# Kernel optimization log

Measured on AMD Instinct MI355X. Metric: run time of the kernel, lower is better.

The kernel has to match this reference:

```python
import jax, jax.numpy as jnp
import numpy as np

N_SAMPLES = 32768
CHANNELS = 128
N_ATOMS = 512
ATOM_SIZE = 512
N_TRANSFERS = 64
TRANSFER_SIZE = 8192
N_EVENTS = 32
N_ROOMS = 8
DILATIONS = (1, 3, 9, 27, 1)
BATCH = 8


def _conv1d(x, w, padding, dil=1):
    # x: [B,C,T], w: [O,I,K]
    return jax.lax.conv_general_dilated(
        x, w, (1,), padding, rhs_dilation=(dil,),
        dimension_numbers=('NCH', 'OIH', 'NCH'))


def _fft_convolve(a, b):
    # linear convolution along last dim, truncated to original length
    n = a.shape[-1]
    af = jnp.fft.rfft(a, n=2 * n)
    bf = jnp.fft.rfft(b, n=2 * n)
    return jnp.fft.irfft(af * bf, n=2 * n)[..., :n]


def _mlp(x, hw, hb, ow, ob):
    # LinearOutputStack: 3 hidden Linear(C,C)+leaky_relu, then Linear(C,out)
    for i in range(hw.shape[0]):
        x = jax.nn.leaky_relu(x @ hw[i] + hb[i], 0.2)
    return x @ ow + ob


def setup_inputs() -> dict:
    key = jax.random.key(0)
    ks = jax.random.split(key, 25)
    s = 0.02
    C = CHANNELS
    return {
        'x': jax.random.normal(ks[0], (BATCH, 1, N_SAMPLES), jnp.float32),
        'bank': jax.random.normal(ks[1], (C, 1, 512), jnp.float32) * s,
        'w_net': jax.random.normal(ks[2], (len(DILATIONS), C, C, 3), jnp.float32) * s,
        'b_net': jnp.zeros((len(DILATIONS), C), jnp.float32),
        'attn_w': jax.random.normal(ks[3], (1, C, 1), jnp.float32) * s,
        'attn_b': jnp.zeros((1,), jnp.float32),
        'atoms_hw': jax.random.normal(ks[4], (3, C, C), jnp.float32) * s,
        'atoms_hb': jnp.zeros((3, C), jnp.float32),
        'atoms_ow': jax.random.normal(ks[5], (C, N_ATOMS), jnp.float32) * s,
        'atoms_ob': jnp.zeros((N_ATOMS,), jnp.float32),
        'trans_hw': jax.random.normal(ks[6], (3, C, C), jnp.float32) * s,
        'trans_hb': jnp.zeros((3, C), jnp.float32),
        'trans_ow': jax.random.normal(ks[7], (C, N_TRANSFERS), jnp.float32) * s,
        'trans_ob': jnp.zeros((N_TRANSFERS,), jnp.float32),
        'amp_hw': jax.random.normal(ks[8], (3, C, C), jnp.float32) * s,
        'amp_hb': jnp.zeros((3, C), jnp.float32),
        'amp_ow': jax.random.normal(ks[9], (C, 1), jnp.float32) * s,
        'amp_ob': jnp.zeros((1,), jnp.float32),
        'atoms_dict': jax.random.uniform(ks[10], (N_ATOMS, ATOM_SIZE), jnp.float32, -1.0, 1.0),
        'transfer_dict': jax.random.normal(ks[11], (N_TRANSFERS, TRANSFER_SIZE), jnp.float32) * 0.01,
        'rooms': jax.random.normal(ks[12], (N_ROOMS, N_SAMPLES), jnp.float32) * 0.01,
        'room_w': jax.random.normal(ks[13], (C, N_ROOMS), jnp.float32) * s,
        'room_b': jnp.zeros((N_ROOMS,), jnp.float32),
        'mix_w': jax.random.normal(ks[14], (C, 1), jnp.float32) * s,
        'mix_b': jnp.zeros((1,), jnp.float32),
    }


def reference(x, bank, w_net, b_net, attn_w, attn_b,
              atoms_hw, atoms_hb, atoms_ow, atoms_ob,
              trans_hw, trans_hb, trans_ow, trans_ob,
              amp_hw, amp_hb, amp_ow, amp_ob,
              atoms_dict, transfer_dict, rooms, room_w, room_b, mix_w, mix_b):
    B = x.shape[0]
    # front-end filter bank, padding=256, truncate to n_samples
    h = _conv1d(x, bank, [(256, 256)])[..., :N_SAMPLES]            # [B,C,T]
    # DilatedStack: residual dilated convs
    for i, d in enumerate(DILATIONS):
        h = h + jax.nn.leaky_relu(
            _conv1d(h, w_net[i], 'SAME', d) + b_net[i][None, :, None], 0.2)
    # ExampleNorm: per-example std normalization
    h = h / (jnp.std(h, axis=(1, 2), keepdims=True) + 1e-8)
    context = jnp.max(h, axis=-1)                                   # [B,C]
    attn = jax.nn.sigmoid(_conv1d(h, attn_w, 'SAME') + attn_b[None, :, None])[:, 0, :]  # [B,T]
    # sparsify_vectors: top-k attention positions, latents scaled by attn
    vals, idx = jax.lax.top_k(attn, N_EVENTS)                        # [B,E]
    lat = jnp.take_along_axis(jnp.swapaxes(h, 1, 2), idx[..., None], axis=1) * vals[..., None]  # [B,E,C]
    atoms = jax.nn.softmax(_mlp(lat, atoms_hw, atoms_hb, atoms_ow, atoms_ob), axis=-1) @ atoms_dict
    transfers = jax.nn.softmax(_mlp(lat, trans_hw, trans_hb, trans_ow, trans_ob), axis=-1) @ transfer_dict
    amps = _mlp(lat, amp_hw, amp_hb, amp_ow, amp_ob) ** 2            # [B,E,1]
    atoms = jnp.pad(atoms, ((0, 0), (0, 0), (0, TRANSFER_SIZE - ATOM_SIZE)))
    ev = (_fft_convolve(atoms, transfers) + atoms) * amps            # [B,E,Ts]
    # overlap-add scatter. NOTE: faithful to the original, which does
    # output[:, :, idx:idx+Ts] += x[i, e] -- every event accumulates into a
    # buffer shared across the whole batch.
    pos = idx.reshape(-1)[:, None] + jnp.arange(TRANSFER_SIZE)[None, :]  # [B*E,Ts]
    buf = jnp.zeros(2 * N_SAMPLES, ev.dtype).at[pos].add(ev.reshape(-1, TRANSFER_SIZE))
    dry = jnp.broadcast_to(buf[:N_SAMPLES][None, :], (B, N_SAMPLES))  # [B,T]
    # ReverbGenerator: context -> room choice + wet/dry mix
    impulse = jax.nn.softmax(context @ room_w + room_b, axis=-1) @ rooms  # [B,T]
    mix = jax.nn.sigmoid(context @ mix_w + mix_b)                     # [B,1]
    wet = _fft_convolve(dry, impulse)
    out = dry * (1.0 - mix) + wet * mix
    return out[:, None, :]
```

## Files before the change

### kernel.cpp

```cpp
#include <hip/hip_runtime.h>
#include <math.h>

#define TSAMP 32768
#define CCH 128
#define NBATCH 8
#define NEV 32
#define NROWS 256
#define NATOMS 512
#define ASIZE 512
#define NTRANS 64
#define TSIZE 8192

#define DRY_SCALE 16777216.0f
#define IMP_SCALE 64.0f
#define WET_DESCALE 9.313225746154785e-10f

#define EPAD(i) ((i) + ((i) >> 5))

typedef _Float16 f16x8 __attribute__((ext_vector_type(8)));
typedef _Float16 f16x4 __attribute__((ext_vector_type(4)));
typedef float f32x4 __attribute__((ext_vector_type(4)));


__global__ void k_zs(double* __restrict__ sums) {
  if (threadIdx.x < 16) sums[threadIdx.x] = 0.0;
}

__global__ __launch_bounds__(256) void k_zero(float* __restrict__ wet,
                                              float* __restrict__ dry) {
  int i = blockIdx.x * 256 + threadIdx.x;
  if (i < NBATCH * TSAMP) wet[i] = 0.f;
  if (i < TSAMP) dry[i] = 0.f;
}

__global__ __launch_bounds__(256) void k_wsplit(const float* __restrict__ wn,
                                                _Float16* __restrict__ whi,
                                                _Float16* __restrict__ wlo) {
  const int i = blockIdx.x * 256 + threadIdx.x;
  if (i >= 245760) return;
  const int ci = i & 127;
  int r = i >> 7;
  const int o = r & 127;
  r >>= 7;
  const int k = r % 3;
  const int l = r / 3;
  const float w = wn[(((size_t)l*128 + o)*128 + ci)*3 + k];
  const _Float16 hi = (_Float16)w;
  whi[i] = hi;
  wlo[i] = (_Float16)(w - (float)hi);
}

__global__ __launch_bounds__(256) void k_bsplit(const float* __restrict__ bank,
                                                _Float16* __restrict__ bhi,
                                                _Float16* __restrict__ blo) {
  const int i = blockIdx.x * 256 + threadIdx.x;
  if (i < 65536) {
    const float w = bank[i];
    const _Float16 hi = (_Float16)w;
    bhi[i] = hi;
    blo[i] = (_Float16)(w - (float)hi);
  }
}

__global__ __launch_bounds__(256) void k_front_mfma(
    const float* __restrict__ x, const _Float16* __restrict__ bhi,
    const _Float16* __restrict__ blo, float* __restrict__ h) {
  __shared__ _Float16 shi[8*664];
  __shared__ _Float16 slo[8*664];
  const int t0 = blockIdx.x * 128;
  const int b  = blockIdx.y;
  const float* xb = x + (size_t)b*TSAMP;
  const int tid = threadIdx.x;

  for (int flat = tid; flat < 8*632; flat += 256) {
    const int p = flat / 632;
    const int q = flat - p*632;
    const int g = t0 - 256 + q + p;
    const float v = (g >= 0 && g < TSAMP) ? xb[g] : 0.f;
    const _Float16 hi = (_Float16)v;
    shi[p*664 + q] = hi;
    slo[p*664 + q] = (_Float16)(v - (float)hi);
  }
  __syncthreads();

  const int wv = tid >> 6;
  const int lane = tid & 63;
  const int n = lane & 15;
  const int quad = lane >> 4;
  const int c0 = wv * 32;
  const int ph = n & 7;
  const int nb = n & 8;

  f32x4 acc[2][8];
#pragma unroll
  for (int i = 0; i < 2; ++i)
#pragma unroll
    for (int j = 0; j < 8; ++j) acc[i][j] = (f32x4){0.f,0.f,0.f,0.f};

  for (int kc = 0; kc < 16; ++kc) {
    const int kb = kc*32 + quad*8;
    f16x8 ahi[2], alo[2];
#pragma unroll
    for (int os = 0; os < 2; ++os) {
      const size_t ao = (size_t)(c0 + os*16 + n)*512 + kb;
      ahi[os] = *(const f16x8*)(bhi + ao);
      alo[os] = *(const f16x8*)(blo + ao);
    }
#pragma unroll
    for (int tg = 0; tg < 2; ++tg) {
      f16x8 xh[4], xl[4];
#pragma unroll
      for (int u = 0; u < 4; ++u) {
        const int a = ph*664 + (tg*4 + u)*16 + nb + kb;
        xh[u] = *(const f16x8*)(shi + a);
        xl[u] = *(const f16x8*)(slo + a);
      }
#pragma unroll
      for (int os = 0; os < 2; ++os)
#pragma unroll
        for (int u = 0; u < 4; ++u) {
          f32x4 a4 = acc[os][tg*4 + u];
          a4 = __builtin_amdgcn_mfma_f32_16x16x32_f16(ahi[os], xh[u], a4, 0, 0, 0);
          a4 = __builtin_amdgcn_mfma_f32_16x16x32_f16(alo[os], xh[u], a4, 0, 0, 0);
          a4 = __builtin_amdgcn_mfma_f32_16x16x32_f16(ahi[os], xl[u], a4, 0, 0, 0);
          acc[os][tg*4 + u] = a4;
        }
    }
  }

  float* hb = h + (size_t)b*TSAMP*CCH;
#pragma unroll
  for (int os = 0; os < 2; ++os) {
    const int cb = c0 + os*16 + quad*4;
#pragma unroll
    for (int ts = 0; ts < 8; ++ts) {
      const int t = t0 + ts*16 + n;
      *(f32x4*)(hb + (size_t)t*CCH + cb) = acc[os][ts];
    }
  }
}

__global__ __launch_bounds__(256) void k_dil_mfma(
    const float* __restrict__ hin0, const _Float16* __restrict__ whi,
    const _Float16* __restrict__ wlo, const float* __restrict__ bias,
    float* __restrict__ hout0, const int d) {
  extern __shared__ _Float16 sh[];
  const int twin = 64 + 2*d;
  _Float16* shi = sh;
  _Float16* slo = sh + twin*136;
  const int t0 = blockIdx.x * 64;
  const size_t bs = (size_t)blockIdx.y * CCH * TSAMP;
  const float* __restrict__ hin = hin0 + bs;
  float* __restrict__ hout = hout0 + bs;
  const int tid = threadIdx.x;

  for (int flat = tid; flat < twin*32; flat += 256) {
    const int tw = flat >> 5;
    const int c4 = (flat & 31) << 2;
    const int g = t0 - d + tw;
    float4 v = {0.f, 0.f, 0.f, 0.f};
    if (g >= 0 && g < TSAMP) v = *(const float4*)(hin + (size_t)g*CCH + c4);
    f16x4 hv, lv;
    hv[0] = (_Float16)v.x; hv[1] = (_Float16)v.y;
    hv[2] = (_Float16)v.z; hv[3] = (_Float16)v.w;
    lv[0] = (_Float16)(v.x - (float)hv[0]); lv[1] = (_Float16)(v.y - (float)hv[1]);
    lv[2] = (_Float16)(v.z - (float)hv[2]); lv[3] = (_Float16)(v.w - (float)hv[3]);
    *(f16x4*)(shi + tw*136 + c4) = hv;
    *(f16x4*)(slo + tw*136 + c4) = lv;
  }
  __syncthreads();

  const int wv = tid >> 6;
  const int lane = tid & 63;
  const int n = lane & 15;
  const int quad = lane >> 4;
  const int o0 = wv * 32;

  f32x4 acc[2][4];
#pragma unroll
  for (int i = 0; i < 2; ++i)
#pragma unroll
    for (int j = 0; j < 4; ++j) acc[i][j] = (f32x4){0.f,0.f,0.f,0.f};

  for (int k = 0; k < 3; ++k) {
    for (int kc = 0; kc < 4; ++kc) {
      const int cib = kc*32 + quad*8;
      f16x8 ahi[2], alo[2];
#pragma unroll
      for (int os = 0; os < 2; ++os) {
        const size_t wo = ((size_t)k*128 + (o0 + os*16 + n))*128 + cib;
        ahi[os] = *(const f16x8*)(whi + wo);
        alo[os] = *(const f16x8*)(wlo + wo);
      }
      f16x8 bhi[4], blo[4];
#pragma unroll
      for (int ts = 0; ts < 4; ++ts) {
        const int a = (ts*16 + n + k*d)*136 + cib;
        bhi[ts] = *(const f16x8*)(shi + a);
        blo[ts] = *(const f16x8*)(slo + a);
      }
#pragma unroll
      for (int os = 0; os < 2; ++os)
#pragma unroll
        for (int ts = 0; ts < 4; ++ts) {
          acc[os][ts] = __builtin_amdgcn_mfma_f32_16x16x32_f16(ahi[os], bhi[ts], acc[os][ts], 0, 0, 0);
          acc[os][ts] = __builtin_amdgcn_mfma_f32_16x16x32_f16(alo[os], bhi[ts], acc[os][ts], 0, 0, 0);
          acc[os][ts] = __builtin_amdgcn_mfma_f32_16x16x32_f16(ahi[os], blo[ts], acc[os][ts], 0, 0, 0);
        }
    }
  }

#pragma unroll
  for (int os = 0; os < 2; ++os) {
    const int ob = o0 + os*16 + quad*4;
    const f32x4 bs4 = *(const f32x4*)(bias + ob);
#pragma unroll
    for (int ts = 0; ts < 4; ++ts) {
      const int t = t0 + ts*16 + n;
      const int tw = ts*16 + n + d;
      const f16x4 phv = *(const f16x4*)(shi + tw*136 + ob);
      const f16x4 plv = *(const f16x4*)(slo + tw*136 + ob);
      f32x4 res;
#pragma unroll
      for (int r = 0; r < 4; ++r) {
        float v = acc[os][ts][r] + bs4[r];
        v = v > 0.f ? v : 0.2f*v;
        res[r] = (float)phv[r] + (float)plv[r] + v;
      }
      *(f32x4*)(hout + (size_t)t*CCH + ob) = res;
    }
  }
}

__global__ __launch_bounds__(256) void k_dil128(
    const float* __restrict__ hin0, const _Float16* __restrict__ whi,
    const _Float16* __restrict__ wlo, const float* __restrict__ bias,
    float* __restrict__ hout0, const int d) {
  extern __shared__ _Float16 sh[];
  const int twin = 128 + 2*d;
  _Float16* shi = sh;
  _Float16* slo = sh + twin*136;
  const int t0 = blockIdx.x * 128;
  const size_t bs = (size_t)blockIdx.y * CCH * TSAMP;
  const float* __restrict__ hin = hin0 + bs;
  float* __restrict__ hout = hout0 + bs;
  const int tid = threadIdx.x;

  for (int flat = tid; flat < twin*32; flat += 256) {
    const int tw = flat >> 5;
    const int c4 = (flat & 31) << 2;
    const int g = t0 - d + tw;
    float4 v = {0.f, 0.f, 0.f, 0.f};
    if (g >= 0 && g < TSAMP) v = *(const float4*)(hin + (size_t)g*CCH + c4);
    f16x4 hv, lv;
    hv[0] = (_Float16)v.x; hv[1] = (_Float16)v.y;
    hv[2] = (_Float16)v.z; hv[3] = (_Float16)v.w;
    lv[0] = (_Float16)(v.x - (float)hv[0]); lv[1] = (_Float16)(v.y - (float)hv[1]);
    lv[2] = (_Float16)(v.z - (float)hv[2]); lv[3] = (_Float16)(v.w - (float)hv[3]);
    *(f16x4*)(shi + tw*136 + c4) = hv;
    *(f16x4*)(slo + tw*136 + c4) = lv;
  }
  __syncthreads();

  const int wv = tid >> 6;
  const int lane = tid & 63;
  const int n = lane & 15;
  const int quad = lane >> 4;
  const int o0 = wv * 32;

  f32x4 acc[2][8];
#pragma unroll
  for (int i = 0; i < 2; ++i)
#pragma unroll
    for (int j = 0; j < 8; ++j) acc[i][j] = (f32x4){0.f,0.f,0.f,0.f};

  for (int k = 0; k < 3; ++k) {
    for (int kc = 0; kc < 4; ++kc) {
      const int cib = kc*32 + quad*8;
      f16x8 ahi[2], alo[2];
#pragma unroll
      for (int os = 0; os < 2; ++os) {
        const size_t wo = ((size_t)k*128 + (o0 + os*16 + n))*128 + cib;
        ahi[os] = *(const f16x8*)(whi + wo);
        alo[os] = *(const f16x8*)(wlo + wo);
      }
#pragma unroll
      for (int tg = 0; tg < 2; ++tg) {
        f16x8 bh[4], bl[4];
#pragma unroll
        for (int u = 0; u < 4; ++u) {
          const int a = ((tg*4 + u)*16 + n + k*d)*136 + cib;
          bh[u] = *(const f16x8*)(shi + a);
          bl[u] = *(const f16x8*)(slo + a);
        }
#pragma unroll
        for (int os = 0; os < 2; ++os)
#pragma unroll
          for (int u = 0; u < 4; ++u) {
            f32x4 a4 = acc[os][tg*4 + u];
            a4 = __builtin_amdgcn_mfma_f32_16x16x32_f16(ahi[os], bh[u], a4, 0, 0, 0);
            a4 = __builtin_amdgcn_mfma_f32_16x16x32_f16(alo[os], bh[u], a4, 0, 0, 0);
            a4 = __builtin_amdgcn_mfma_f32_16x16x32_f16(ahi[os], bl[u], a4, 0, 0, 0);
            acc[os][tg*4 + u] = a4;
          }
      }
    }
  }

#pragma unroll
  for (int os = 0; os < 2; ++os) {
    const int ob = o0 + os*16 + quad*4;
    const f32x4 bs4 = *(const f32x4*)(bias + ob);
#pragma unroll
    for (int ts = 0; ts < 8; ++ts) {
      const int t = t0 + ts*16 + n;
      const int tw = ts*16 + n + d;
      const f16x4 phv = *(const f16x4*)(shi + tw*136 + ob);
      const f16x4 plv = *(const f16x4*)(slo + tw*136 + ob);
      f32x4 res;
#pragma unroll
      for (int r = 0; r < 4; ++r) {
        float v = acc[os][ts][r] + bs4[r];
        v = v > 0.f ? v : 0.2f*v;
        res[r] = (float)phv[r] + (float)plv[r] + v;
      }
      *(f32x4*)(hout + (size_t)t*CCH + ob) = res;
    }
  }
}

__global__ __launch_bounds__(256) void k_dil_last(
    const float* __restrict__ hin0, const _Float16* __restrict__ whi,
    const _Float16* __restrict__ wlo, const float* __restrict__ bias,
    float* __restrict__ hout0, const int d,
    const float* __restrict__ aw, double* __restrict__ sums,
    float* __restrict__ attnraw, float* __restrict__ pm, const int bb0) {
  extern __shared__ _Float16 sh[];
  const int twin = 128 + 2*d;
  _Float16* shi = sh;
  _Float16* slo = sh + twin*136;
  __shared__ float attl[4*128];
  __shared__ double sred[8];
  const int t0 = blockIdx.x * 128;
  const int b = bb0 + blockIdx.y;
  const size_t bs = (size_t)blockIdx.y * CCH * TSAMP;
  const float* __restrict__ hin = hin0 + bs;
  float* __restrict__ hout = hout0 + bs;
  const int tid = threadIdx.x;

  for (int flat = tid; flat < twin*32; flat += 256) {
    const int tw = flat >> 5;
    const int c4 = (flat & 31) << 2;
    const int g = t0 - d + tw;
    float4 v = {0.f, 0.f, 0.f, 0.f};
    if (g >= 0 && g < TSAMP) v = *(const float4*)(hin + (size_t)g*CCH + c4);
    f16x4 hv, lv;
    hv[0] = (_Float16)v.x; hv[1] = (_Float16)v.y;
    hv[2] = (_Float16)v.z; hv[3] = (_Float16)v.w;
    lv[0] = (_Float16)(v.x - (float)hv[0]); lv[1] = (_Float16)(v.y - (float)hv[1]);
    lv[2] = (_Float16)(v.z - (float)hv[2]); lv[3] = (_Float16)(v.w - (float)hv[3]);
    *(f16x4*)(shi + tw*136 + c4) = hv;
    *(f16x4*)(slo + tw*136 + c4) = lv;
  }
  __syncthreads();

  const int wv = tid >> 6;
  const int lane = tid & 63;
  const int n = lane & 15;
  const int quad = lane >> 4;
  const int o0 = wv * 32;

  f32x4 acc[2][8];
#pragma unroll
  for (int i = 0; i < 2; ++i)
#pragma unroll
    for (int j = 0; j < 8; ++j) acc[i][j] = (f32x4){0.f,0.f,0.f,0.f};

  for (int k = 0; k < 3; ++k) {
    for (int kc = 0; kc < 4; ++kc) {
      const int cib = kc*32 + quad*8;
      f16x8 ahi[2], alo[2];
#pragma unroll
      for (int os = 0; os < 2; ++os) {
        const size_t wo = ((size_t)k*128 + (o0 + os*16 + n))*128 + cib;
        ahi[os] = *(const f16x8*)(whi + wo);
        alo[os] = *(const f16x8*)(wlo + wo);
      }
#pragma unroll
      for (int tg = 0; tg < 2; ++tg) {
        f16x8 bh[4], bl[4];
#pragma unroll
        for (int u = 0; u < 4; ++u) {
          const int a = ((tg*4 + u)*16 + n + k*d)*136 + cib;
          bh[u] = *(const f16x8*)(shi + a);
          bl[u] = *(const f16x8*)(slo + a);
        }
#pragma unroll
        for (int os = 0; os < 2; ++os)
#pragma unroll
          for (int u = 0; u < 4; ++u) {
            f32x4 a4 = acc[os][tg*4 + u];
            a4 = __builtin_amdgcn_mfma_f32_16x16x32_f16(ahi[os], bh[u], a4, 0, 0, 0);
            a4 = __builtin_amdgcn_mfma_f32_16x16x32_f16(alo[os], bh[u], a4, 0, 0, 0);
            a4 = __builtin_amdgcn_mfma_f32_16x16x32_f16(ahi[os], bl[u], a4, 0, 0, 0);
            acc[os][tg*4 + u] = a4;
          }
      }
    }
  }

  const f32x4 awq0 = *(const f32x4*)(aw + o0 + quad*4);
  const f32x4 awq1 = *(const f32x4*)(aw + o0 + 16 + quad*4);
  double s = 0.0, s2 = 0.0;
  float pa[8] = {0.f,0.f,0.f,0.f,0.f,0.f,0.f,0.f};
  f32x4 cm[2];
  cm[0] = (f32x4){-3.4e38f, -3.4e38f, -3.4e38f, -3.4e38f};
  cm[1] = cm[0];

#pragma unroll
  for (int os = 0; os < 2; ++os) {
    const int ob = o0 + os*16 + quad*4;
    const f32x4 bs4 = *(const f32x4*)(bias + ob);
    const f32x4 awv = os ? awq1 : awq0;
#pragma unroll
    for (int ts = 0; ts < 8; ++ts) {
      const int t = t0 + ts*16 + n;
      const int tw = ts*16 + n + d;
      const f16x4 phv = *(const f16x4*)(shi + tw*136 + ob);
      const f16x4 plv = *(const f16x4*)(slo + tw*136 + ob);
      f32x4 res;
      float dotp = 0.f;
#pragma unroll
      for (int r = 0; r < 4; ++r) {
        float v = acc[os][ts][r] + bs4[r];
        v = v > 0.f ? v : 0.2f*v;
        const float hv = (float)phv[r] + (float)plv[r] + v;
        res[r] = hv;
        s += (double)hv; s2 += (double)hv*(double)hv;
        dotp += hv * awv[r];
        cm[os][r] = fmaxf(cm[os][r], hv);
      }
      pa[ts] += dotp;
      *(f32x4*)(hout + (size_t)t*CCH + ob) = res;
    }
  }

#pragma unroll
  for (int ts = 0; ts < 8; ++ts) {
    pa[ts] += __shfl_xor(pa[ts], 16);
    pa[ts] += __shfl_xor(pa[ts], 32);
  }
  if (quad == 0) {
#pragma unroll
    for (int ts = 0; ts < 8; ++ts) attl[wv*128 + ts*16 + n] = pa[ts];
  }
#pragma unroll
  for (int mk = 1; mk <= 8; mk <<= 1)
#pragma unroll
    for (int os = 0; os < 2; ++os)
#pragma unroll
      for (int r = 0; r < 4; ++r)
        cm[os][r] = fmaxf(cm[os][r], __shfl_xor(cm[os][r], mk));
  if (n == 0) {
#pragma unroll
    for (int os = 0; os < 2; ++os)
      *(f32x4*)(pm + ((size_t)b*256 + blockIdx.x)*128 + o0 + os*16 + quad*4) = cm[os];
  }
  for (int sft = 32; sft; sft >>= 1) { s += __shfl_down(s, sft); s2 += __shfl_down(s2, sft); }
  if (lane == 0) { sred[wv*2] = s; sred[wv*2+1] = s2; }
  __syncthreads();
  if (tid < 128)
    attnraw[(size_t)b*TSAMP + t0 + tid] =
        attl[tid] + attl[128 + tid] + attl[256 + tid] + attl[384 + tid];
  if (tid == 0) {
    atomicAdd(&sums[b*2],   sred[0] + sred[2] + sred[4] + sred[6]);
    atomicAdd(&sums[b*2+1], sred[1] + sred[3] + sred[5] + sred[7]);
  }
}

__global__ void k_scale(const double* __restrict__ sums, float* __restrict__ scal) {
  const int b = threadIdx.x;
  if (b < NBATCH) {
    const double n = (double)CCH * (double)TSAMP;
    const double mean = sums[b*2] / n;
    double var = sums[b*2+1] / n - mean*mean;
    if (var < 0.0) var = 0.0;
    scal[b] = (float)(1.0 / (sqrt(var) + 1e-8));
  }
}

__global__ void k_context2(const float* __restrict__ pm, const float* __restrict__ scal,
                           float* __restrict__ ctx) {
  const int b = blockIdx.x;
  const int c = threadIdx.x;
  float m = -3.4e38f;
  for (int s = 0; s < 256; ++s) m = fmaxf(m, pm[((size_t)b*256 + s)*128 + c]);
  ctx[b*128 + c] = m * scal[b];
}

__global__ __launch_bounds__(256) void k_topk1(const float* __restrict__ raw,
                                               const float* __restrict__ scal,
                                               const float* __restrict__ ab,
                                               float* __restrict__ cv,
                                               int* __restrict__ cidx) {
  const int ch = blockIdx.x, b = blockIdx.y;
  const float sc = scal[b], bb_ = ab[0];
  const float* a = raw + (size_t)b*TSAMP + ch*2048;
  __shared__ float v[2048];
  __shared__ float rv[4]; __shared__ int ri[4];
  const int tid = threadIdx.x;
  for (int i = tid; i < 2048; i += 256)
    v[i] = 1.f/(1.f+expf(-(a[i]*sc + bb_)));
  __syncthreads();
  for (int e = 0; e < NEV; ++e) {
    float bv = -1e30f; int bi = 0;
    for (int i = tid; i < 2048; i += 256) {
      const float x = v[i];
      if (x > bv) { bv = x; bi = i; }
    }
    for (int s = 32; s; s >>= 1) {
      const float ov = __shfl_down(bv, s); const int oi = __shfl_down(bi, s);
      if (ov > bv || (ov == bv && oi < bi)) { bv = ov; bi = oi; }
    }
    if ((tid & 63) == 0) { rv[tid >> 6] = bv; ri[tid >> 6] = bi; }
    __syncthreads();
    if (tid == 0) {
      int bb = 0;
      for (int w2 = 1; w2 < 4; ++w2)
        if (rv[w2] > rv[bb] || (rv[w2] == rv[bb] && ri[w2] < ri[bb])) bb = w2;
      cv[(b*16 + ch)*NEV + e] = rv[bb];
      cidx[(b*16 + ch)*NEV + e] = ch*2048 + ri[bb];
      v[ri[bb]] = -1e30f;
    }
    __syncthreads();
  }
}

__global__ __launch_bounds__(512) void k_topk2(const float* __restrict__ cv,
                                               const int* __restrict__ ci_,
                                               float* __restrict__ vals,
                                               int* __restrict__ idxs) {
  const int b = blockIdx.x;
  const int tid = threadIdx.x;
  float my = cv[b*512 + tid];
  int   mi = ci_[b*512 + tid];
  __shared__ float rv[8]; __shared__ int ri[8];
  __shared__ float bvs; __shared__ int bis;
  for (int e = 0; e < NEV; ++e) {
    float bv = my; int bi = mi;
    for (int s = 32; s; s >>= 1) {
      const float ov = __shfl_down(bv, s); const int oi = __shfl_down(bi, s);
      if (ov > bv || (ov == bv && oi < bi)) { bv = ov; bi = oi; }
    }
    if ((tid & 63) == 0) { rv[tid >> 6] = bv; ri[tid >> 6] = bi; }
    __syncthreads();
    if (tid == 0) {
      int bb = 0;
      for (int w2 = 1; w2 < 8; ++w2)
        if (rv[w2] > rv[bb] || (rv[w2] == rv[bb] && ri[w2] < ri[bb])) bb = w2;
      vals[b*NEV + e] = rv[bb]; idxs[b*NEV + e] = ri[bb];
      bvs = rv[bb]; bis = ri[bb];
    }
    __syncthreads();
    if (mi == bis && my == bvs) my = -1e30f;
    __syncthreads();
  }
}

__device__ __forceinline__ float blk_max128(float v, float* red) {
  const int tid = threadIdx.x;
  red[tid] = v; __syncthreads();
  for (int s = 64; s > 0; s >>= 1) {
    if (tid < s) red[tid] = fmaxf(red[tid], red[tid + s]);
    __syncthreads();
  }
  const float r = red[0]; __syncthreads();
  return r;
}
__device__ __forceinline__ float blk_sum128(float v, float* red) {
  const int tid = threadIdx.x;
  red[tid] = v; __syncthreads();
  for (int s = 64; s > 0; s >>= 1) {
    if (tid < s) red[tid] += red[tid + s];
    __syncthreads();
  }
  const float r = red[0]; __syncthreads();
  return r;
}
__device__ __forceinline__ float mlp_hidden3(float latv, const float* __restrict__ hw,
                                             const float* __restrict__ hb, float* xa) {
  const int tid = threadIdx.x;
  float cur = latv;
  for (int i = 0; i < 3; ++i) {
    xa[tid] = cur; __syncthreads();
    const float* W = hw + (size_t)i*CCH*CCH;
    float acc = hb[i*CCH + tid];
    for (int c = 0; c < CCH; ++c) acc += xa[c] * W[c*CCH + tid];
    cur = acc > 0.f ? acc : 0.2f*acc;
    __syncthreads();
  }
  return cur;
}

__global__ __launch_bounds__(128) void k_mlp(
    const float* __restrict__ h, const float* __restrict__ scal,
    const float* __restrict__ vals, const int* __restrict__ idxs,
    const float* __restrict__ a_hw, const float* __restrict__ a_hb,
    const float* __restrict__ a_ow, const float* __restrict__ a_ob,
    const float* __restrict__ t_hw, const float* __restrict__ t_hb,
    const float* __restrict__ t_ow, const float* __restrict__ t_ob,
    const float* __restrict__ m_hw, const float* __restrict__ m_hb,
    const float* __restrict__ m_ow, const float* __restrict__ m_ob,
    float* __restrict__ p_atoms, float* __restrict__ p_trans, float* __restrict__ amps) {
  const int row = blockIdx.x;
  const int b = row >> 5;
  const int tid = threadIdx.x;
  __shared__ float xa[CCH];
  __shared__ float red[CCH];
  const int t = idxs[row];
  const float latv = h[((size_t)b*TSAMP + t)*CCH + tid] * scal[b] * vals[row];

  {
    const float cur = mlp_hidden3(latv, a_hw, a_hb, xa);
    xa[tid] = cur; __syncthreads();
    float l0 = a_ob[tid], l1 = a_ob[tid+128], l2 = a_ob[tid+256], l3 = a_ob[tid+384];
    for (int c = 0; c < CCH; ++c) {
      const float xv = xa[c];
      const float* W = a_ow + (size_t)c*NATOMS + tid;
      l0 += xv*W[0]; l1 += xv*W[128]; l2 += xv*W[256]; l3 += xv*W[384];
    }
    const float mx = blk_max128(fmaxf(fmaxf(l0,l1), fmaxf(l2,l3)), red);
    const float e0 = expf(l0-mx), e1 = expf(l1-mx), e2 = expf(l2-mx), e3 = expf(l3-mx);
    const float inv = 1.f / blk_sum128(e0+e1+e2+e3, red);
    float* pa = p_atoms + (size_t)row*NATOMS;
    pa[tid] = e0*inv; pa[tid+128] = e1*inv; pa[tid+256] = e2*inv; pa[tid+384] = e3*inv;
  }
  {
    const float cur = mlp_hidden3(latv, t_hw, t_hb, xa);
    xa[tid] = cur; __syncthreads();
    float lg = -3.4e38f;
    if (tid < NTRANS) {
      float acc = t_ob[tid];
      for (int c = 0; c < CCH; ++c) acc += xa[c]*t_ow[c*NTRANS + tid];
      lg = acc;
    }
    const float mt = blk_max128(lg, red);
    const float et = (tid < NTRANS) ? expf(lg - mt) : 0.f;
    const float st = blk_sum128(et, red);
    if (tid < NTRANS) p_trans[(size_t)row*NTRANS + tid] = et/st;
  }
  {
    const float cur = mlp_hidden3(latv, m_hw, m_hb, xa);
    const float s = blk_sum128(cur * m_ow[tid], red);
    if (tid == 0) { const float v = s + m_ob[0]; amps[row] = v*v; }
  }
}

__global__ __launch_bounds__(256) void k_atoms_mm(const float* __restrict__ p_atoms,
                                                  const float* __restrict__ dict,
                                                  float* __restrict__ av) {
  const int row = blockIdx.x;
  __shared__ float p[NATOMS];
  for (int i = threadIdx.x; i < NATOMS; i += 256) p[i] = p_atoms[(size_t)row*NATOMS + i];
  __syncthreads();
  const int s0 = threadIdx.x*2;
  float a0=0, a1=0;
  for (int a = 0; a < NATOMS; ++a) {
    const float pa = p[a];
    const float2 dv = *(const float2*)(dict + (size_t)a*ASIZE + s0);
    a0 += pa*dv.x; a1 += pa*dv.y;
  }
  av[(size_t)row*ASIZE + s0] = a0; av[(size_t)row*ASIZE + s0 + 1] = a1;
}

__global__ __launch_bounds__(256) void k_trans_mm(const float* __restrict__ p_trans,
                                                   const float* __restrict__ td,
                                                   float* __restrict__ trans) {
  const int row = blockIdx.y;
  const int t = blockIdx.x*2048 + threadIdx.x*8;
  __shared__ float p[NTRANS];
  if (threadIdx.x < NTRANS) p[threadIdx.x] = p_trans[(size_t)row*NTRANS + threadIdx.x];
  __syncthreads();
  float a0=0,a1=0,a2=0,a3=0,a4=0,a5=0,a6=0,a7=0;
  for (int j = 0; j < NTRANS; ++j) {
    const float pj = p[j];
    const float4 v0 = *(const float4*)(td + (size_t)j*TSIZE + t);
    const float4 v1 = *(const float4*)(td + (size_t)j*TSIZE + t + 4);
    a0 += pj*v0.x; a1 += pj*v0.y; a2 += pj*v0.z; a3 += pj*v0.w;
    a4 += pj*v1.x; a5 += pj*v1.y; a6 += pj*v1.z; a7 += pj*v1.w;
  }
  float* o = trans + (size_t)row*TSIZE + t;
  o[0]=a0; o[1]=a1; o[2]=a2; o[3]=a3; o[4]=a4; o[5]=a5; o[6]=a6; o[7]=a7;
}

__global__ __launch_bounds__(256) void k_ev(const float* __restrict__ trans,
                                            const float* __restrict__ av,
                                            const float* __restrict__ amps,
                                            float* __restrict__ ev) {
  const int row = blockIdx.y;
  const int t0 = blockIdx.x * 1024;
  __shared__ float al[512];
  __shared__ float tw[1584];
  for (int i = threadIdx.x; i < 512; i += 256) al[i] = av[(size_t)row*ASIZE + i];
  for (int i = threadIdx.x; i < 1536; i += 256) {
    const int g = t0 - 512 + i;
    tw[EPAD(i)] = (g >= 0) ? trans[(size_t)row*TSIZE + g] : 0.f;
  }
  __syncthreads();
  const int base = threadIdx.x*4 + 512;
  float a0=0,a1=0,a2=0,a3=0;
  float w0=tw[EPAD(base)], w1=tw[EPAD(base+1)], w2=tw[EPAD(base+2)], w3=tw[EPAD(base+3)];
#pragma unroll 8
  for (int k = 0; k < 512; ++k) {
    const float ak = al[k];
    a0 += ak*w0; a1 += ak*w1; a2 += ak*w2; a3 += ak*w3;
    w3 = w2; w2 = w1; w1 = w0;
    const int p = base - k - 1;
    w0 = tw[EPAD(p)];
  }
  const int n = t0 + threadIdx.x*4;
  const float amp = amps[row];
  float* e = ev + (size_t)row*TSIZE + n;
  e[0] = (a0 + (n+0 < 512 ? al[n+0] : 0.f)) * amp;
  e[1] = (a1 + (n+1 < 512 ? al[n+1] : 0.f)) * amp;
  e[2] = (a2 + (n+2 < 512 ? al[n+2] : 0.f)) * amp;
  e[3] = (a3 + (n+3 < 512 ? al[n+3] : 0.f)) * amp;
}

__global__ __launch_bounds__(256) void k_dry(const float* __restrict__ ev,
                                             const int* __restrict__ idxs,
                                             float* __restrict__ dry) {
  __shared__ int sidx[32];
  const int r0 = blockIdx.y * 32;
  if (threadIdx.x < 32) sidx[threadIdx.x] = idxs[r0 + threadIdx.x];
  __syncthreads();
  const int p = blockIdx.x*512 + threadIdx.x*2;
  float a0=0,a1=0;
  for (int r = 0; r < 32; ++r) {
    const int off = p - sidx[r];
    if (off >= -1 && off < TSIZE) {
      const float* er = ev + (size_t)(r0 + r)*TSIZE;
      if ((unsigned)(off  ) < TSIZE) a0 += er[off];
      if ((unsigned)(off+1) < TSIZE) a1 += er[off+1];
    }
  }
  atomicAdd(dry + p,     a0);
  atomicAdd(dry + p + 1, a1);
}

__global__ __launch_bounds__(256) void k_dryrev(const float* __restrict__ dry,
                                                _Float16* __restrict__ drev) {
  const int i = blockIdx.x*256 + threadIdx.x;
  if (i < TSAMP + 1088)
    drev[i] = (i < TSAMP) ? (_Float16)(dry[TSAMP-1-i] * DRY_SCALE) : (_Float16)0.f;
}

__global__ void k_room(const float* __restrict__ ctx, const float* __restrict__ room_w,
                       const float* __restrict__ room_b, const float* __restrict__ mix_w,
                       const float* __restrict__ mix_b, float* __restrict__ roomp,
                       float* __restrict__ mix) {
  const int b = threadIdx.x >> 3;
  const int r = threadIdx.x & 7;
  float acc = room_b[r];
  for (int c = 0; c < CCH; ++c) acc += ctx[b*CCH + c] * room_w[c*8 + r];
  float m = acc;
  for (int s = 1; s < 8; s <<= 1) m = fmaxf(m, __shfl_xor(m, s, 8));
  const float e = expf(acc - m);
  float ssum = e;
  for (int s = 1; s < 8; s <<= 1) ssum += __shfl_xor(ssum, s, 8);
  roomp[b*8 + r] = e / ssum;
  if (r == 0) {
    float a = mix_b[0];
    for (int c = 0; c < CCH; ++c) a += ctx[b*CCH + c] * mix_w[c];
    mix[b] = 1.f/(1.f+expf(-a));
  }
}

__global__ __launch_bounds__(256) void k_impulse(const float* __restrict__ roomp,
                                                 const float* __restrict__ rooms,
                                                 _Float16* __restrict__ ihi) {
  const int b = blockIdx.y;
  const int t = blockIdx.x*1024 + threadIdx.x*4;
  float a0=0,a1=0,a2=0,a3=0;
  for (int r = 0; r < 8; ++r) {
    const float pr = roomp[b*8 + r];
    const float4 v = *(const float4*)(rooms + (size_t)r*TSAMP + t);
    a0 += pr*v.x; a1 += pr*v.y; a2 += pr*v.z; a3 += pr*v.w;
  }
  _Float16* oh = ihi + (size_t)b*TSAMP + t;
  oh[0] = (_Float16)(a0*IMP_SCALE); oh[1] = (_Float16)(a1*IMP_SCALE);
  oh[2] = (_Float16)(a2*IMP_SCALE); oh[3] = (_Float16)(a3*IMP_SCALE);
}

__global__ __launch_bounds__(256) void k_wet_mfma(
    const _Float16* __restrict__ drev, const _Float16* __restrict__ ihi,
    float* __restrict__ wet) {
  const int t0 = blockIdx.x * 512;
  const int k0 = blockIdx.y * 4096;
  if (k0 > t0 + 511) return;
  __shared__ _Float16 rhi[8*1048];
  const int tid = threadIdx.x;
  const int wv = tid >> 6;
  const int lane = tid & 63;
  const int n16 = lane & 15;
  const int quad = lane >> 4;
  const int m = n16;

  f32x4 acc[8];
#pragma unroll
  for (int j = 0; j < 8; ++j) acc[j] = (f32x4){0.f,0.f,0.f,0.f};

  const int kend = (k0 + 4096 < t0 + 512) ? k0 + 4096 : t0 + 512;
  const int ph = 7 - (n16 & 7);
  for (int kc0 = k0; kc0 < kend; kc0 += 512) {
    const int RB = TSAMP - 1 - (t0 + 511 - kc0);
    for (int flat = tid; flat < 8*1016; flat += 256) {
      const int p = flat / 1016;
      const int q = flat - p*1016;
      rhi[p*1048 + q] = drev[RB + p + q];
    }
    __syncthreads();

#pragma unroll 4
    for (int kc = 0; kc < 16; ++kc) {
      const int kb = kc*32;
      const int jg = kc0 + kb + quad*8;
      f16x8 ah;
      if (m < NBATCH) ah = *(const f16x8*)(ihi + (size_t)m*TSAMP + jg);
      else ah = (f16x8){0,0,0,0,0,0,0,0};
#pragma unroll
      for (int ts = 0; ts < 8; ++ts) {
        const int nn = wv*128 + ts*16 + n16;
        const int a = ph*1048 + kb + quad*8 + 504 - (nn & ~7);
        const f16x8 bh = *(const f16x8*)(rhi + a);
        acc[ts] = __builtin_amdgcn_mfma_f32_16x16x32_f16(ah, bh, acc[ts], 0, 0, 0);
      }
    }
    __syncthreads();
  }

#pragma unroll
  for (int ts = 0; ts < 8; ++ts) {
    const int t = t0 + wv*128 + ts*16 + n16;
#pragma unroll
    for (int r = 0; r < 4; ++r) {
      const int b = quad*4 + r;
      if (b < NBATCH)
        atomicAdd(wet + (size_t)b*TSAMP + t, acc[ts][r] * WET_DESCALE);
    }
  }
}

__global__ __launch_bounds__(256) void k_out(const float* __restrict__ dry,
                                             const float* __restrict__ wet,
                                             const float* __restrict__ mix,
                                             float* __restrict__ out) {
  const int b = blockIdx.y;
  const int t = blockIdx.x*1024 + threadIdx.x*4;
  const float m = mix[b];
  const float4 d = *(const float4*)(dry + t);
  const float4 w = *(const float4*)(wet + (size_t)b*TSAMP + t);
  float* o = out + (size_t)b*TSAMP + t;
  o[0] = d.x*(1.f-m) + w.x*m;
  o[1] = d.y*(1.f-m) + w.y*m;
  o[2] = d.z*(1.f-m) + w.z*m;
  o[3] = d.w*(1.f-m) + w.w*m;
}

extern "C" void kernel_launch(void* const* d_in, const int* in_sizes, int n_in,
                              void* d_out, int out_size, void* d_ws, size_t ws_size,
                              hipStream_t stream) {
  (void)in_sizes; (void)n_in; (void)out_size; (void)ws_size;
  const float* x      = (const float*)d_in[0];
  const float* bank   = (const float*)d_in[1];
  const float* w_net  = (const float*)d_in[2];
  const float* b_net  = (const float*)d_in[3];
  const float* attn_w = (const float*)d_in[4];
  const float* attn_b = (const float*)d_in[5];
  const float* a_hw = (const float*)d_in[6];
  const float* a_hb = (const float*)d_in[7];
  const float* a_ow = (const float*)d_in[8];
  const float* a_ob = (const float*)d_in[9];
  const float* t_hw = (const float*)d_in[10];
  const float* t_hb = (const float*)d_in[11];
  const float* t_ow = (const float*)d_in[12];
  const float* t_ob = (const float*)d_in[13];
  const float* m_hw = (const float*)d_in[14];
  const float* m_hb = (const float*)d_in[15];
  const float* m_ow = (const float*)d_in[16];
  const float* m_ob = (const float*)d_in[17];
  const float* atoms_dict    = (const float*)d_in[18];
  const float* transfer_dict = (const float*)d_in[19];
  const float* rooms  = (const float*)d_in[20];
  const float* room_w = (const float*)d_in[21];
  const float* room_b = (const float*)d_in[22];
  const float* mix_w  = (const float*)d_in[23];
  const float* mix_b  = (const float*)d_in[24];
  float* out = (float*)d_out;

  float* ws = (float*)d_ws;
  float* H  = ws;
  float* t1 = ws + (size_t)33554432;
  float* t2 = ws + (size_t)41943040;
  _Float16* whi = (_Float16*)(ws + (size_t)50331648);
  _Float16* wlo = (_Float16*)(ws + (size_t)50454528);
  _Float16* bhi = (_Float16*)(ws + (size_t)50577408);
  _Float16* blo = (_Float16*)(ws + (size_t)50610176);
  double* sums  = (double*)(ws + (size_t)50642944);
  float* attnraw = ws + (size_t)50642976;
  float* pm      = ws + (size_t)50905120;

  size_t off = 33554432;
  float* scal  = ws + off; off += 8;
  float* ctx   = ws + off; off += NBATCH*CCH;
  float* vals  = ws + off; off += NROWS;
  int*   idxs  = (int*)(ws + off); off += NROWS;
  float* p_atoms = ws + off; off += (size_t)NROWS*NATOMS;
  float* p_trans = ws + off; off += (size_t)NROWS*NTRANS;
  float* amps  = ws + off; off += NROWS;
  float* av    = ws + off; off += (size_t)NROWS*ASIZE;
  float* trans = ws + off; off += (size_t)NROWS*TSIZE;
  float* ev    = ws + off; off += (size_t)NROWS*TSIZE;
  float* dry   = ws + off; off += TSAMP;
  float* roomp = ws + off; off += 64;
  float* mix   = ws + off; off += 8;
  float* wet   = ws + off; off += (size_t)NBATCH*TSAMP;
  float* cand_v = ws + off; off += 4096;
  int*   cand_i = (int*)(ws + off); off += 4096;
  _Float16* imphi = (_Float16*)(ws + off); off += (size_t)NBATCH*TSAMP/2;
  _Float16* drev  = (_Float16*)(ws + off); off += (TSAMP + 1088)/2 + 4;

  k_zs<<<1, 64, 0, stream>>>(sums);
  k_wsplit<<<960, 256, 0, stream>>>(w_net, whi, wlo);
  k_bsplit<<<256, 256, 0, stream>>>(bank, bhi, blo);
  k_front_mfma<<<dim3(256, 8), 256, 0, stream>>>(x, bhi, blo, H);

  const int dil[5] = {1, 3, 9, 27, 1};
  const size_t S = (size_t)CCH * TSAMP;
  for (int p = 0; p < 4; ++p) {
    float* Hp = H + (size_t)(2*p) * S;
    float* io[6] = {Hp, t1, t2, t1, t2, Hp};
    for (int i = 0; i < 3; ++i) {
      const int d = dil[i];
      const size_t smem = (size_t)(128 + 2*d) * 544;
      k_dil128<<<dim3(256, 2), 256, smem, stream>>>(
          io[i], whi + (size_t)i*49152, wlo + (size_t)i*49152, b_net + i*CCH,
          io[i+1], d);
    }
    {
      const int d = dil[3];
      const size_t smem = (size_t)(64 + 2*d) * 544;
      k_dil_mfma<<<dim3(512, 2), 256, smem, stream>>>(
          io[3], whi + (size_t)3*49152, wlo + (size_t)3*49152, b_net + 3*CCH,
          io[4], d);
    }
    {
      const int d = dil[4];
      const size_t smem = (size_t)(128 + 2*d) * 544;
      k_dil_last<<<dim3(256, 2), 256, smem, stream>>>(
          io[4], whi + (size_t)4*49152, wlo + (size_t)4*49152, b_net + 4*CCH,
          io[5], d, attn_w, sums, attnraw, pm, 2*p);
    }
  }

  k_zero<<<1024, 256, 0, stream>>>(wet, dry);
  k_scale<<<1, 64, 0, stream>>>(sums, scal);
  k_context2<<<8, 128, 0, stream>>>(pm, scal, ctx);
  k_topk1<<<dim3(16, 8), 256, 0, stream>>>(attnraw, scal, attn_b, cand_v, cand_i);
  k_topk2<<<8, 512, 0, stream>>>(cand_v, cand_i, vals, idxs);
  k_mlp<<<256, 128, 0, stream>>>(H, scal, vals, idxs,
                                 a_hw, a_hb, a_ow, a_ob,
                                 t_hw, t_hb, t_ow, t_ob,
                                 m_hw, m_hb, m_ow, m_ob,
                                 p_atoms, p_trans, amps);
  k_atoms_mm<<<256, 256, 0, stream>>>(p_atoms, atoms_dict, av);
  k_trans_mm<<<dim3(4, 256), 256, 0, stream>>>(p_trans, transfer_dict, trans);
  k_ev<<<dim3(8, 256), 256, 0, stream>>>(trans, av, amps, ev);
  k_dry<<<dim3(64, 8), 256, 0, stream>>>(ev, idxs, dry);
  k_dryrev<<<133, 256, 0, stream>>>(dry, drev);
  k_room<<<1, 64, 0, stream>>>(ctx, room_w, room_b, mix_w, mix_b, roomp, mix);
  k_impulse<<<dim3(32, 8), 256, 0, stream>>>(roomp, rooms, imphi);
  k_wet_mfma<<<dim3(64, 8), 256, 0, stream>>>(drev, imphi, wet);
  k_out<<<dim3(32, 8), 256, 0, stream>>>(dry, wet, mix, out);
}
```

Baseline: 1.210 ms.

## Fuse small launches, widen batch chunking, retile dilation-27 conv to 80 steps

Merges the weight/bank split and sum-zeroing kernels into one launch, and folds the scale, context and room/mix kernels into a single finisher kernel. The dry scatter now gathers over all 256 events without atomics and writes the reversed fp16 buffer directly, removing a separate kernel and the dry zeroing. When the workspace is large enough, the dilated stack processes 4 batch items per launch instead of 2, halving the launch count for the conv chain. The d=27 conv uses an 80-step tile to reduce halo overhead, at the cost of a bounds check and more registers.

```diff
diff --git a/kernel.cpp b/kernel.cpp
--- a/kernel.cpp
+++ b/kernel.cpp
@@ -22,44 +22,40 @@
 typedef float f32x4 __attribute__((ext_vector_type(4)));
 
 
-__global__ void k_zs(double* __restrict__ sums) {
-  if (threadIdx.x < 16) sums[threadIdx.x] = 0.0;
+__global__ __launch_bounds__(256) void k_prep(const float* __restrict__ wn,
+                                              const float* __restrict__ bank,
+                                              _Float16* __restrict__ whi,
+                                              _Float16* __restrict__ wlo,
+                                              _Float16* __restrict__ bhi,
+                                              _Float16* __restrict__ blo,
+                                              double* __restrict__ sums) {
+  const int i = blockIdx.x * 256 + threadIdx.x;
+  if (i < 16) sums[i] = 0.0;
+  if (i < 245760) {
+    const int ci = i & 127;
+    int r = i >> 7;
+    const int o = r & 127;
+    r >>= 7;
+    const int k = r % 3;
+    const int l = r / 3;
+    const float w = wn[(((size_t)l*128 + o)*128 + ci)*3 + k];
+    const _Float16 hi = (_Float16)w;
+    whi[i] = hi;
+    wlo[i] = (_Float16)(w - (float)hi);
+  } else if (i < 311296) {
+    const int j = i - 245760;
+    const float w = bank[j];
+    const _Float16 hi = (_Float16)w;
+    bhi[j] = hi;
+    blo[j] = (_Float16)(w - (float)hi);
+  }
 }
 
 __global__ __launch_bounds__(256) void k_zero(float* __restrict__ wet,
-                                              float* __restrict__ dry) {
+                                              _Float16* __restrict__ drev) {
   int i = blockIdx.x * 256 + threadIdx.x;
   if (i < NBATCH * TSAMP) wet[i] = 0.f;
-  if (i < TSAMP) dry[i] = 0.f;
-}
-
-__global__ __launch_bounds__(256) void k_wsplit(const float* __restrict__ wn,
-                                                _Float16* __restrict__ whi,
-                                                _Float16* __restrict__ wlo) {
-  const int i = blockIdx.x * 256 + threadIdx.x;
-  if (i >= 245760) return;
-  const int ci = i & 127;
-  int r = i >> 7;
-  const int o = r & 127;
-  r >>= 7;
-  const int k = r % 3;
-  const int l = r / 3;
-  const float w = wn[(((size_t)l*128 + o)*128 + ci)*3 + k];
-  const _Float16 hi = (_Float16)w;
-  whi[i] = hi;
-  wlo[i] = (_Float16)(w - (float)hi);
-}
-
-__global__ __launch_bounds__(256) void k_bsplit(const float* __restrict__ bank,
-                                                _Float16* __restrict__ bhi,
-                                                _Float16* __restrict__ blo) {
-  const int i = blockIdx.x * 256 + threadIdx.x;
-  if (i < 65536) {
-    const float w = bank[i];
-    const _Float16 hi = (_Float16)w;
-    bhi[i] = hi;
-    blo[i] = (_Float16)(w - (float)hi);
-  }
+  if (i < 1088) drev[TSAMP + i] = (_Float16)0.f;
 }
 
 __global__ __launch_bounds__(256) void k_front_mfma(
@@ -140,15 +136,16 @@
   }
 }
 
-__global__ __launch_bounds__(256) void k_dil_mfma(
+__global__ __launch_bounds__(256) void k_dil80(
     const float* __restrict__ hin0, const _Float16* __restrict__ whi,
     const _Float16* __restrict__ wlo, const float* __restrict__ bias,
-    float* __restrict__ hout0, const int d) {
+    float* __restrict__ hout0) {
+  const int d = 27;
   extern __shared__ _Float16 sh[];
-  const int twin = 64 + 2*d;
+  const int twin = 80 + 2*d;
   _Float16* shi = sh;
   _Float16* slo = sh + twin*136;
-  const int t0 = blockIdx.x * 64;
+  const int t0 = blockIdx.x * 80;
   const size_t bs = (size_t)blockIdx.y * CCH * TSAMP;
   const float* __restrict__ hin = hin0 + bs;
   float* __restrict__ hout = hout0 + bs;
@@ -176,11 +173,11 @@
   const int quad = lane >> 4;
   const int o0 = wv * 32;
 
-  f32x4 acc[2][4];
+  f32x4 acc[2][5];
 #pragma unroll
   for (int i = 0; i < 2; ++i)
 #pragma unroll
-    for (int j = 0; j < 4; ++j) acc[i][j] = (f32x4){0.f,0.f,0.f,0.f};
+    for (int j = 0; j < 5; ++j) acc[i][j] = (f32x4){0.f,0.f,0.f,0.f};
 
   for (int k = 0; k < 3; ++k) {
     for (int kc = 0; kc < 4; ++kc) {
@@ -192,20 +189,20 @@
         ahi[os] = *(const f16x8*)(whi + wo);
         alo[os] = *(const f16x8*)(wlo + wo);
       }
-      f16x8 bhi[4], blo[4];
-#pragma unroll
-      for (int ts = 0; ts < 4; ++ts) {
+      f16x8 bh[5], bl[5];
+#pragma unroll
+      for (int ts = 0; ts < 5; ++ts) {
         const int a = (ts*16 + n + k*d)*136 + cib;
-        bhi[ts] = *(const f16x8*)(shi + a);
-        blo[ts] = *(const f16x8*)(slo + a);
+        bh[ts] = *(const f16x8*)(shi + a);
+        bl[ts] = *(const f16x8*)(slo + a);
       }
 #pragma unroll
       for (int os = 0; os < 2; ++os)
 #pragma unroll
-        for (int ts = 0; ts < 4; ++ts) {
-          acc[os][ts] = __builtin_amdgcn_mfma_f32_16x16x32_f16(ahi[os], bhi[ts], acc[os][ts], 0, 0, 0);
-          acc[os][ts] = __builtin_amdgcn_mfma_f32_16x16x32_f16(alo[os], bhi[ts], acc[os][ts], 0, 0, 0);
-          acc[os][ts] = __builtin_amdgcn_mfma_f32_16x16x32_f16(ahi[os], blo[ts], acc[os][ts], 0, 0, 0);
+        for (int ts = 0; ts < 5; ++ts) {
+          acc[os][ts] = __builtin_amdgcn_mfma_f32_16x16x32_f16(ahi[os], bh[ts], acc[os][ts], 0, 0, 0);
+          acc[os][ts] = __builtin_amdgcn_mfma_f32_16x16x32_f16(alo[os], bh[ts], acc[os][ts], 0, 0, 0);
+          acc[os][ts] = __builtin_amdgcn_mfma_f32_16x16x32_f16(ahi[os], bl[ts], acc[os][ts], 0, 0, 0);
         }
     }
   }
@@ -215,19 +212,21 @@
     const int ob = o0 + os*16 + quad*4;
     const f32x4 bs4 = *(const f32x4*)(bias + ob);
 #pragma unroll
-    for (int ts = 0; ts < 4; ++ts) {
+    for (int ts = 0; ts < 5; ++ts) {
       const int t = t0 + ts*16 + n;
-      const int tw = ts*16 + n + d;
-      const f16x4 phv = *(const f16x4*)(shi + tw*136 + ob);
-      const f16x4 plv = *(const f16x4*)(slo + tw*136 + ob);
-      f32x4 res;
-#pragma unroll
-      for (int r = 0; r < 4; ++r) {
-        float v = acc[os][ts][r] + bs4[r];
-        v = v > 0.f ? v : 0.2f*v;
-        res[r] = (float)phv[r] + (float)plv[r] + v;
-      }
-      *(f32x4*)(hout + (size_t)t*CCH + ob) = res;
+      if (t < TSAMP) {
+        const int tw = ts*16 + n + d;
+        const f16x4 phv = *(const f16x4*)(shi + tw*136 + ob);
+        const f16x4 plv = *(const f16x4*)(slo + tw*136 + ob);
+        f32x4 res;
+#pragma unroll
+        for (int r = 0; r < 4; ++r) {
+          float v = acc[os][ts][r] + bs4[r];
+          v = v > 0.f ? v : 0.2f*v;
+          res[r] = (float)phv[r] + (float)plv[r] + v;
+        }
+        *(f32x4*)(hout + (size_t)t*CCH + ob) = res;
+      }
     }
   }
 }
@@ -478,24 +477,44 @@
   }
 }
 
-__global__ void k_scale(const double* __restrict__ sums, float* __restrict__ scal) {
-  const int b = threadIdx.x;
-  if (b < NBATCH) {
-    const double n = (double)CCH * (double)TSAMP;
-    const double mean = sums[b*2] / n;
-    double var = sums[b*2+1] / n - mean*mean;
+__global__ __launch_bounds__(128) void k_finish(
+    const double* __restrict__ sums, const float* __restrict__ pm,
+    const float* __restrict__ room_w, const float* __restrict__ room_b,
+    const float* __restrict__ mix_w, const float* __restrict__ mix_b,
+    float* __restrict__ scal, float* __restrict__ roomp, float* __restrict__ mix) {
+  const int b = blockIdx.x;
+  const int tid = threadIdx.x;
+  __shared__ float bs;
+  __shared__ float ctx[128];
+  if (tid == 0) {
+    const double nn = (double)CCH * (double)TSAMP;
+    const double mean = sums[b*2] / nn;
+    double var = sums[b*2+1] / nn - mean*mean;
     if (var < 0.0) var = 0.0;
-    scal[b] = (float)(1.0 / (sqrt(var) + 1e-8));
-  }
-}
-
-__global__ void k_context2(const float* __restrict__ pm, const float* __restrict__ scal,
-                           float* __restrict__ ctx) {
-  const int b = blockIdx.x;
-  const int c = threadIdx.x;
+    const float sc = (float)(1.0 / (sqrt(var) + 1e-8));
+    bs = sc;
+    scal[b] = sc;
+  }
+  __syncthreads();
   float m = -3.4e38f;
-  for (int s = 0; s < 256; ++s) m = fmaxf(m, pm[((size_t)b*256 + s)*128 + c]);
-  ctx[b*128 + c] = m * scal[b];
+  for (int s = 0; s < 256; ++s) m = fmaxf(m, pm[((size_t)b*256 + s)*128 + tid]);
+  ctx[tid] = m * bs;
+  __syncthreads();
+  if (tid < 8) {
+    const int r = tid;
+    float acc = room_b[r];
+    for (int c = 0; c < CCH; ++c) acc += ctx[c] * room_w[c*8 + r];
+    float mm = acc;
+    for (int s = 1; s < 8; s <<= 1) mm = fmaxf(mm, __shfl_xor(mm, s, 8));
+    const float e = expf(acc - mm);
+    float ss = e;
+    for (int s = 1; s < 8; s <<= 1) ss += __shfl_xor(ss, s, 8);
+    roomp[b*8 + r] = e / ss;
+  } else if (tid == 8) {
+    float a = mix_b[0];
+    for (int c = 0; c < CCH; ++c) a += ctx[c] * mix_w[c];
+    mix[b] = 1.f/(1.f+expf(-a));
+  }
 }
 
 __global__ __launch_bounds__(256) void k_topk1(const float* __restrict__ raw,
@@ -729,51 +748,19 @@
 
 __global__ __launch_bounds__(256) void k_dry(const float* __restrict__ ev,
                                              const int* __restrict__ idxs,
-                                             float* __restrict__ dry) {
-  __shared__ int sidx[32];
-  const int r0 = blockIdx.y * 32;
-  if (threadIdx.x < 32) sidx[threadIdx.x] = idxs[r0 + threadIdx.x];
-  __syncthreads();
-  const int p = blockIdx.x*512 + threadIdx.x*2;
-  float a0=0,a1=0;
-  for (int r = 0; r < 32; ++r) {
+                                             float* __restrict__ dry,
+                                             _Float16* __restrict__ drev) {
+  __shared__ int sidx[NROWS];
+  if (threadIdx.x < NROWS) sidx[threadIdx.x] = idxs[threadIdx.x];
+  __syncthreads();
+  const int p = blockIdx.x*256 + threadIdx.x;
+  float a = 0.f;
+  for (int r = 0; r < NROWS; ++r) {
     const int off = p - sidx[r];
-    if (off >= -1 && off < TSIZE) {
-      const float* er = ev + (size_t)(r0 + r)*TSIZE;
-      if ((unsigned)(off  ) < TSIZE) a0 += er[off];
-      if ((unsigned)(off+1) < TSIZE) a1 += er[off+1];
-    }
-  }
-  atomicAdd(dry + p,     a0);
-  atomicAdd(dry + p + 1, a1);
-}
-
-__global__ __launch_bounds__(256) void k_dryrev(const float* __restrict__ dry,
-                                                _Float16* __restrict__ drev) {
-  const int i = blockIdx.x*256 + threadIdx.x;
-  if (i < TSAMP + 1088)
-    drev[i] = (i < TSAMP) ? (_Float16)(dry[TSAMP-1-i] * DRY_SCALE) : (_Float16)0.f;
-}
-
-__global__ void k_room(const float* __restrict__ ctx, const float* __restrict__ room_w,
-                       const float* __restrict__ room_b, const float* __restrict__ mix_w,
-                       const float* __restrict__ mix_b, float* __restrict__ roomp,
-                       float* __restrict__ mix) {
-  const int b = threadIdx.x >> 3;
-  const int r = threadIdx.x & 7;
-  float acc = room_b[r];
-  for (int c = 0; c < CCH; ++c) acc += ctx[b*CCH + c] * room_w[c*8 + r];
-  float m = acc;
-  for (int s = 1; s < 8; s <<= 1) m = fmaxf(m, __shfl_xor(m, s, 8));
-  const float e = expf(acc - m);
-  float ssum = e;
-  for (int s = 1; s < 8; s <<= 1) ssum += __shfl_xor(ssum, s, 8);
-  roomp[b*8 + r] = e / ssum;
-  if (r == 0) {
-    float a = mix_b[0];
-    for (int c = 0; c < CCH; ++c) a += ctx[b*CCH + c] * mix_w[c];
-    mix[b] = 1.f/(1.f+expf(-a));
-  }
+    if ((unsigned)off < TSIZE) a += ev[(size_t)r*TSIZE + off];
+  }
+  dry[p] = a;
+  drev[TSAMP - 1 - p] = (_Float16)(a * DRY_SCALE);
 }
 
 __global__ __launch_bounds__(256) void k_impulse(const float* __restrict__ roomp,
@@ -870,7 +857,7 @@
 extern "C" void kernel_launch(void* const* d_in, const int* in_sizes, int n_in,
                               void* d_out, int out_size, void* d_ws, size_t ws_size,
                               hipStream_t stream) {
-  (void)in_sizes; (void)n_in; (void)out_size; (void)ws_size;
+  (void)in_sizes; (void)n_in; (void)out_size;
   const float* x      = (const float*)d_in[0];
   const float* bank   = (const float*)d_in[1];
   const float* w_net  = (const float*)d_in[2];
@@ -899,20 +886,23 @@
   float* out = (float*)d_out;
 
   float* ws = (float*)d_ws;
+  const size_t need4 = (size_t)67944480 * 4;
+  const int NB = (ws_size >= need4) ? 4 : 2;
+  const size_t S = (size_t)CCH * TSAMP;
   float* H  = ws;
   float* t1 = ws + (size_t)33554432;
-  float* t2 = ws + (size_t)41943040;
-  _Float16* whi = (_Float16*)(ws + (size_t)50331648);
-  _Float16* wlo = (_Float16*)(ws + (size_t)50454528);
-  _Float16* bhi = (_Float16*)(ws + (size_t)50577408);
-  _Float16* blo = (_Float16*)(ws + (size_t)50610176);
-  double* sums  = (double*)(ws + (size_t)50642944);
-  float* attnraw = ws + (size_t)50642976;
-  float* pm      = ws + (size_t)50905120;
+  float* t2 = ws + 33554432 + NB*S;
+  const size_t w_off = 33554432 + 2*(size_t)NB*S;
+  _Float16* whi = (_Float16*)(ws + w_off);
+  _Float16* wlo = whi + 245760;
+  _Float16* bhi = wlo + 245760;
+  _Float16* blo = bhi + 65536;
+  double* sums  = (double*)(ws + w_off + 311296);
+  float* attnraw = ws + w_off + 311296 + 32;
+  float* pm      = attnraw + (size_t)NBATCH*TSAMP;
 
   size_t off = 33554432;
   float* scal  = ws + off; off += 8;
-  float* ctx   = ws + off; off += NBATCH*CCH;
   float* vals  = ws + off; off += NROWS;
   int*   idxs  = (int*)(ws + off); off += NROWS;
   float* p_atoms = ws + off; off += (size_t)NROWS*NATOMS;
@@ -930,42 +920,39 @@
   _Float16* imphi = (_Float16*)(ws + off); off += (size_t)NBATCH*TSAMP/2;
   _Float16* drev  = (_Float16*)(ws + off); off += (TSAMP + 1088)/2 + 4;
 
-  k_zs<<<1, 64, 0, stream>>>(sums);
-  k_wsplit<<<960, 256, 0, stream>>>(w_net, whi, wlo);
-  k_bsplit<<<256, 256, 0, stream>>>(bank, bhi, blo);
+  k_prep<<<1216, 256, 0, stream>>>(w_net, bank, whi, wlo, bhi, blo, sums);
   k_front_mfma<<<dim3(256, 8), 256, 0, stream>>>(x, bhi, blo, H);
 
   const int dil[5] = {1, 3, 9, 27, 1};
-  const size_t S = (size_t)CCH * TSAMP;
-  for (int p = 0; p < 4; ++p) {
-    float* Hp = H + (size_t)(2*p) * S;
+  const int npairs = 8 / NB;
+  for (int p = 0; p < npairs; ++p) {
+    float* Hp = H + (size_t)(NB*p) * S;
     float* io[6] = {Hp, t1, t2, t1, t2, Hp};
     for (int i = 0; i < 3; ++i) {
       const int d = dil[i];
       const size_t smem = (size_t)(128 + 2*d) * 544;
-      k_dil128<<<dim3(256, 2), 256, smem, stream>>>(
+      k_dil128<<<dim3(256, NB), 256, smem, stream>>>(
           io[i], whi + (size_t)i*49152, wlo + (size_t)i*49152, b_net + i*CCH,
           io[i+1], d);
     }
     {
-      const int d = dil[3];
-      const size_t smem = (size_t)(64 + 2*d) * 544;
-      k_dil_mfma<<<dim3(512, 2), 256, smem, stream>>>(
+      const size_t smem = (size_t)134 * 544;
+      k_dil80<<<dim3(410, NB), 256, smem, stream>>>(
           io[3], whi + (size_t)3*49152, wlo + (size_t)3*49152, b_net + 3*CCH,
-          io[4], d);
+          io[4]);
     }
     {
       const int d = dil[4];
       const size_t smem = (size_t)(128 + 2*d) * 544;
-      k_dil_last<<<dim3(256, 2), 256, smem, stream>>>(
+      k_dil_last<<<dim3(256, NB), 256, smem, stream>>>(
           io[4], whi + (size_t)4*49152, wlo + (size_t)4*49152, b_net + 4*CCH,
-          io[5], d, attn_w, sums, attnraw, pm, 2*p);
-    }
-  }
-
-  k_zero<<<1024, 256, 0, stream>>>(wet, dry);
-  k_scale<<<1, 64, 0, stream>>>(sums, scal);
-  k_context2<<<8, 128, 0, stream>>>(pm, scal, ctx);
+          io[5], d, attn_w, sums, attnraw, pm, NB*p);
+    }
+  }
+
+  k_zero<<<1024, 256, 0, stream>>>(wet, drev);
+  k_finish<<<8, 128, 0, stream>>>(sums, pm, room_w, room_b, mix_w, mix_b,
+                                  scal, roomp, mix);
   k_topk1<<<dim3(16, 8), 256, 0, stream>>>(attnraw, scal, attn_b, cand_v, cand_i);
   k_topk2<<<8, 512, 0, stream>>>(cand_v, cand_i, vals, idxs);
   k_mlp<<<256, 128, 0, stream>>>(H, scal, vals, idxs,
@@ -976,9 +963,7 @@
   k_atoms_mm<<<256, 256, 0, stream>>>(p_atoms, atoms_dict, av);
   k_trans_mm<<<dim3(4, 256), 256, 0, stream>>>(p_trans, transfer_dict, trans);
   k_ev<<<dim3(8, 256), 256, 0, stream>>>(trans, av, amps, ev);
-  k_dry<<<dim3(64, 8), 256, 0, stream>>>(ev, idxs, dry);
-  k_dryrev<<<133, 256, 0, stream>>>(dry, drev);
-  k_room<<<1, 64, 0, stream>>>(ctx, room_w, room_b, mix_w, mix_b, roomp, mix);
+  k_dry<<<128, 256, 0, stream>>>(ev, idxs, dry, drev);
   k_impulse<<<dim3(32, 8), 256, 0, stream>>>(roomp, rooms, imphi);
   k_wet_mfma<<<dim3(64, 8), 256, 0, stream>>>(drev, imphi, wet);
   k_out<<<dim3(32, 8), 256, 0, stream>>>(dry, wet, mix, out);
```

Result: no change. 1.205 ms (-0.4%).
